# Kernel optimization log

Hardware: AMD Instinct MI355X
Metric: run time of the kernel (lower is better)

Reference implementation:

```python
import jax, jax.numpy as jnp
import numpy as np
import math

D_MODEL = 1024
N_HEADS = 16
D_HEAD = D_MODEL // N_HEADS


def setup_inputs() -> dict:
    key = jax.random.key(0)
    k_x, k_wqkv, k_bqkv, k_wp, k_bp = jax.random.split(key, 5)
    B, T = 2, 2048
    s = 1.0 / math.sqrt(D_MODEL)
    return {
        "x": jax.random.normal(k_x, (B, T, D_MODEL), dtype=jnp.float32),
        "W_qkv": jax.random.uniform(k_wqkv, (D_MODEL, 3 * D_MODEL), minval=-s, maxval=s, dtype=jnp.float32),
        "b_qkv": jax.random.uniform(k_bqkv, (3 * D_MODEL,), minval=-s, maxval=s, dtype=jnp.float32),
        "W_proj": jax.random.uniform(k_wp, (D_MODEL, D_MODEL), minval=-s, maxval=s, dtype=jnp.float32),
        "b_proj": jax.random.uniform(k_bp, (D_MODEL,), minval=-s, maxval=s, dtype=jnp.float32),
    }


def reference(x, W_qkv, b_qkv, W_proj, b_proj):
    B, T, C = x.shape
    qkv = x @ W_qkv + b_qkv                      # [B,T,3C]
    qkv = qkv.reshape(B, T, 3, N_HEADS, D_HEAD)
    qkv = jnp.transpose(qkv, (2, 0, 3, 1, 4))     # [3,B,H,T,dh]
    q, k, v = qkv[0], qkv[1], qkv[2]
    scale = math.sqrt(D_HEAD)
    attn = jnp.einsum('bhqd,bhkd->bhqk', q, k) / scale  # [B,H,T,T]
    causal = jnp.tril(jnp.ones((T, T), dtype=bool))
    attn = jnp.where(causal, attn, -jnp.inf)
    attn = jax.nn.softmax(attn, axis=-1)
    out = jnp.einsum('bhqk,bhkd->bhqd', attn, v)  # [B,H,T,dh]
    out = jnp.transpose(out, (0, 2, 1, 3)).reshape(B, T, C)
    return out @ W_proj + b_proj
```

## Files before the change

### kernel.cpp

```cpp
#include <hip/hip_runtime.h>

#define B_    2
#define T_    2048
#define C_    1024
#define H_    16
#define DH_   64
#define M_    (B_ * T_)
#define NQKV  (3 * C_)

typedef __bf16 bf16;
typedef __bf16 bf16x4 __attribute__((ext_vector_type(4)));
typedef __bf16 bf16x8 __attribute__((ext_vector_type(8)));
typedef float  f32x4  __attribute__((ext_vector_type(4)));

__device__ __forceinline__ void async16(const void* g, void* l) {
  __builtin_amdgcn_global_load_lds(
      (const __attribute__((address_space(1))) void*)g,
      (__attribute__((address_space(3))) void*)l, 16, 0, 0);
}

__global__ __launch_bounds__(256) void cvt_bf16_k(const float* __restrict__ in,
                                                  bf16* __restrict__ out) {
  const int i = (blockIdx.x * 256 + threadIdx.x) * 4;
  float4 v = *(const float4*)(in + i);
  bf16x4 o;
  o[0] = (bf16)v.x; o[1] = (bf16)v.y; o[2] = (bf16)v.z; o[3] = (bf16)v.w;
  *(bf16x4*)(out + i) = o;
}

__global__ __launch_bounds__(256) void transpose_cvt(const float* __restrict__ in,
                                                     bf16* __restrict__ out,
                                                     int R, int C) {
  __shared__ float tile[32][33];
  const int c0 = blockIdx.x * 32, r0 = blockIdx.y * 32;
  const int tx = threadIdx.x, ty = threadIdx.y;
#pragma unroll
  for (int j = 0; j < 4; j++)
    tile[ty + j * 8][tx] = in[(size_t)(r0 + ty + j * 8) * C + c0 + tx];
  __syncthreads();
#pragma unroll
  for (int j = 0; j < 4; j++)
    out[(size_t)(c0 + ty + j * 8) * R + r0 + tx] = (bf16)tile[tx][ty + j * 8];
}

template <int EPI, int BM>
__global__ __launch_bounds__(256) void gemm_k(
    const bf16* __restrict__ A, const bf16* __restrict__ Bt,
    const float* __restrict__ bias, float* __restrict__ outF,
    bf16* __restrict__ qb, bf16* __restrict__ kb, bf16* __restrict__ vtb) {
  constexpr int K = 1024;
  constexpr int MI = BM / 32;
  __shared__ alignas(16) bf16 As[BM * 64];
  __shared__ alignas(16) bf16 Bs[128 * 64];
  const int tid = threadIdx.x;
  const int lane = tid & 63, wv = tid >> 6;
  const int l15 = lane & 15, quad = lane >> 4;
  const int wm = (wv >> 1) * (BM / 2), wn = (wv & 1) * 64;
  const int m0 = blockIdx.x * BM, n0 = blockIdx.y * 128;

  f32x4 acc[MI][4] = {};

  const int srow = tid >> 3;
  const int sgb = ((tid & 7) ^ (srow & 7)) * 8;
  const bf16* ga = A + (size_t)(m0 + srow) * K + sgb;
  const bf16* gb = Bt + (size_t)(n0 + srow) * K + sgb;
  const int swz = l15 & 7;

  for (int it = 0; it < K / 64; ++it) {
    const int k0 = it * 64;
#pragma unroll
    for (int c = 0; c < BM / 32; c++)
      async16(ga + k0 + (size_t)(c * 32) * K, As + tid * 8 + c * 2048);
#pragma unroll
    for (int c = 0; c < 4; c++)
      async16(gb + k0 + (size_t)(c * 32) * K, Bs + tid * 8 + c * 2048);
    __syncthreads();
    bf16x8 af[2][MI], bfr[2][4];
#pragma unroll
    for (int kb = 0; kb < 2; kb++) {
#pragma unroll
      for (int i = 0; i < MI; i++)
        af[kb][i] = *(const bf16x8*)(As + (wm + i * 16 + l15) * 64 +
                                     (((kb * 4 + quad) ^ swz) << 3));
#pragma unroll
      for (int j = 0; j < 4; j++)
        bfr[kb][j] = *(const bf16x8*)(Bs + (wn + j * 16 + l15) * 64 +
                                      (((kb * 4 + quad) ^ swz) << 3));
    }
#pragma unroll
    for (int kb = 0; kb < 2; kb++)
#pragma unroll
      for (int i = 0; i < MI; i++)
#pragma unroll
        for (int j = 0; j < 4; j++)
          acc[i][j] = __builtin_amdgcn_mfma_f32_16x16x32_bf16(
              af[kb][i], bfr[kb][j], acc[i][j], 0, 0, 0);
    __syncthreads();
  }

#pragma unroll
  for (int i = 0; i < MI; i++) {
#pragma unroll
    for (int j = 0; j < 4; j++) {
      const int gcol = n0 + wn + j * 16 + l15;
      const float bv = bias[gcol];
#pragma unroll
      for (int r = 0; r < 4; r++) {
        const int grow = m0 + wm + i * 16 + quad * 4 + r;
        float v = acc[i][j][r] + bv;
        if constexpr (EPI == 0) {
          const int which = gcol >> 10;
          const int hn = gcol & 1023;
          const int h = hn >> 6, d = hn & 63;
          const int bb = grow >> 11, t = grow & 2047;
          const int head = bb * 16 + h;
          if (which == 0)
            qb[head * 131072 + t * 64 + d] = (bf16)(v * 0.1803368801f);
          else if (which == 1)
            kb[head * 131072 + t * 64 + d] = (bf16)v;
          else
            vtb[head * 131072 + d * 2048 + t] = (bf16)v;
        } else {
          outF[(size_t)grow * 1024 + gcol] = v;
        }
      }
    }
  }
}

__global__ __launch_bounds__(512, 2) void attn_k(const bf16* __restrict__ Q,
                                                 const bf16* __restrict__ K,
                                                 const bf16* __restrict__ Vt,
                                                 bf16* __restrict__ O) {
  __shared__ alignas(16) bf16 Ks[2][128 * 64];
  __shared__ alignas(16) bf16 Vs[2][64 * 128];
  __shared__ alignas(16) bf16 Ps[8][16 * 128];
  const int tid = threadIdx.x, lane = tid & 63, wv = tid >> 6;
  const int l15 = lane & 15, quad = lane >> 4;

  const int b = blockIdx.x;
  const int bh = (b & 7) | ((b >> 6) << 3);
  const int xpair = (b >> 3) & 7;

  const bf16* Qb = Q + (size_t)bh * 131072;
  const bf16* Kb = K + (size_t)bh * 131072;
  const bf16* Vb = Vt + (size_t)bh * 131072;

  const int krow = tid >> 3;
  const int kg = (tid & 7) ^ (krow & 7);
  const bf16* gk = Kb + krow * 64 + kg * 8;
  const int vrow = tid >> 4;
  const int vg = (tid & 15) ^ (vrow & 15);
  const bf16* gv = Vb + vrow * 2048 + vg * 8;

  const int swz7 = l15 & 7;
  bf16* Pw = Ps[wv];
  const int bb = bh >> 4, h = bh & 15;

  for (int t = 0; t < 2; ++t) {
    const int qJ = t ? (15 - xpair) : xpair;
    const int q0 = qJ * 128;
    const int nIter = qJ + 1;
    const int q = q0 + wv * 16 + l15;

    bf16x8 aq0 = *(const bf16x8*)(Qb + q * 64 + quad * 8);
    bf16x8 aq1 = *(const bf16x8*)(Qb + q * 64 + 32 + quad * 8);

    f32x4 o[4] = {};
    float m = -3.0e38f, lsum = 0.f;

    __syncthreads();
    async16(gk, &Ks[0][tid * 8]);
    async16(gk + 64 * 64, &Ks[0][tid * 8 + 4096]);
    async16(gv, &Vs[0][tid * 8]);
    async16(gv + 32 * 2048, &Vs[0][tid * 8 + 4096]);

    for (int it = 0; it < nIter; ++it) {
      __syncthreads();
      const bf16* Kc = Ks[it & 1];
      const bf16* Vc = Vs[it & 1];

      bf16x8 kf[2][8];
#pragma unroll
      for (int kc = 0; kc < 2; kc++)
#pragma unroll
        for (int nf = 0; nf < 8; nf++)
          kf[kc][nf] = *(const bf16x8*)(Kc + (nf * 16 + l15) * 64 +
                                        (((kc * 4 + quad) ^ swz7) << 3));

      if (it + 1 < nIter) {
        const int kt1 = (it + 1) * 128;
        const int nb = (it + 1) & 1;
        async16(gk + kt1 * 64, &Ks[nb][tid * 8]);
        async16(gk + kt1 * 64 + 64 * 64, &Ks[nb][tid * 8 + 4096]);
        async16(gv + kt1, &Vs[nb][tid * 8]);
        async16(gv + kt1 + 32 * 2048, &Vs[nb][tid * 8 + 4096]);
      }

      f32x4 s[8] = {};
#pragma unroll
      for (int kc = 0; kc < 2; kc++) {
        bf16x8 a = kc ? aq1 : aq0;
#pragma unroll
        for (int nf = 0; nf < 8; nf++)
          s[nf] = __builtin_amdgcn_mfma_f32_16x16x32_bf16(kf[kc][nf], a, s[nf], 0, 0, 0);
      }

      if (it == nIter - 1) {
#pragma unroll
        for (int nf = 0; nf < 8; nf++)
#pragma unroll
          for (int r = 0; r < 4; r++) {
            const int kt = it * 128 + nf * 16 + quad * 4 + r;
            if (kt > q) s[nf][r] = -3.0e38f;
          }
      }

      float mx = s[0][0];
#pragma unroll
      for (int nf = 0; nf < 8; nf++)
#pragma unroll
        for (int r = 0; r < 4; r++) mx = fmaxf(mx, s[nf][r]);
      mx = fmaxf(mx, __shfl_xor(mx, 16));
      mx = fmaxf(mx, __shfl_xor(mx, 32));
      const float mnew = fmaxf(m, mx);
      const float alpha = __builtin_amdgcn_exp2f(m - mnew);
      m = mnew;
      float ts = 0.f;
      bf16x4 p4[8];
#pragma unroll
      for (int nf = 0; nf < 8; nf++)
#pragma unroll
        for (int r = 0; r < 4; r++) {
          const float pv = __builtin_amdgcn_exp2f(s[nf][r] - mnew);
          ts += pv;
          p4[nf][r] = (bf16)pv;
        }
      ts += __shfl_xor(ts, 16);
      ts += __shfl_xor(ts, 32);
      lsum = lsum * alpha + ts;
#pragma unroll
      for (int nf = 0; nf < 4; nf++)
#pragma unroll
        for (int r = 0; r < 4; r++) o[nf][r] *= alpha;

#pragma unroll
      for (int nf = 0; nf < 8; nf++)
        *(bf16x4*)(Pw + l15 * 128 + ((((nf << 1) | (quad >> 1)) ^ l15) << 3) +
                   ((quad & 1) << 2)) = p4[nf];

      bf16x8 pb[4];
#pragma unroll
      for (int kc = 0; kc < 4; kc++)
        pb[kc] = *(const bf16x8*)(Pw + l15 * 128 + (((kc * 4 + quad) ^ l15) << 3));

#pragma unroll
      for (int kc = 0; kc < 4; kc++)
#pragma unroll
        for (int nf = 0; nf < 4; nf++) {
          bf16x8 vf = *(const bf16x8*)(Vc + (nf * 16 + l15) * 128 +
                                       (((kc * 4 + quad) ^ l15) << 3));
          o[nf] = __builtin_amdgcn_mfma_f32_16x16x32_bf16(vf, pb[kc], o[nf], 0, 0, 0);
        }
    }

    const float inv = 1.0f / lsum;
#pragma unroll
    for (int nf = 0; nf < 4; nf++) {
      bf16x4 ov;
#pragma unroll
      for (int r = 0; r < 4; r++) ov[r] = (bf16)(o[nf][r] * inv);
      *(bf16x4*)(O + (size_t)(bb * 2048 + q) * 1024 + h * 64 + nf * 16 + quad * 4) = ov;
    }
  }
}

extern "C" void kernel_launch(void* const* d_in, const int* in_sizes, int n_in,
                              void* d_out, int out_size, void* d_ws, size_t ws_size,
                              hipStream_t stream) {
  const float* x     = (const float*)d_in[0];
  const float* Wqkv  = (const float*)d_in[1];
  const float* bqkv  = (const float*)d_in[2];
  const float* Wproj = (const float*)d_in[3];
  const float* bproj = (const float*)d_in[4];
  float* out = (float*)d_out;

  char* p = (char*)d_ws;
  bf16* xbf    = (bf16*)p; p += (size_t)M_ * C_ * 2;
  bf16* wqkvT  = (bf16*)p; p += (size_t)NQKV * C_ * 2;
  bf16* wprojT = (bf16*)p; p += (size_t)C_ * C_ * 2;
  bf16* Qb     = (bf16*)p; p += (size_t)M_ * C_ * 2;
  bf16* Kb     = (bf16*)p; p += (size_t)M_ * C_ * 2;
  bf16* Vtb    = (bf16*)p; p += (size_t)M_ * C_ * 2;
  bf16* AO     = (bf16*)p;

  cvt_bf16_k<<<M_ * C_ / 1024, 256, 0, stream>>>(x, xbf);
  transpose_cvt<<<dim3(NQKV / 32, C_ / 32), dim3(32, 8), 0, stream>>>(Wqkv, wqkvT, C_, NQKV);
  transpose_cvt<<<dim3(C_ / 32, C_ / 32), dim3(32, 8), 0, stream>>>(Wproj, wprojT, C_, C_);

  gemm_k<0, 128><<<dim3(M_ / 128, NQKV / 128), 256, 0, stream>>>(
      xbf, wqkvT, bqkv, nullptr, Qb, Kb, Vtb);

  attn_k<<<256, 512, 0, stream>>>(Qb, Kb, Vtb, AO);

  gemm_k<1, 64><<<dim3(M_ / 64, C_ / 128), 256, 0, stream>>>(
      AO, wprojT, bproj, out, nullptr, nullptr, nullptr);
}
```

Baseline: 173.0 us.

## Split attention blocks per query tile and shrink LDS for higher occupancy

The attention kernel now launches one block per query tile instead of looping over a paired tile, doubling the grid and dropping the balanced-pair loop. LDS use is cut by single-buffering K (with an extra barrier mid-QK so the next K tile can be prefetched after the first half of the dot product) and by halving the per-wave P staging buffer, which is processed in two halves. Launch bounds ask for 4 blocks per CU to raise occupancy. The cost is an extra barrier per iteration, less K prefetch overlap, and tighter register limits that may cause spills. Work per block is also less balanced across blocks than with the paired scheme.

```diff
diff --git a/kernel.cpp b/kernel.cpp
--- a/kernel.cpp
+++ b/kernel.cpp
@@ -77,24 +77,24 @@
     __syncthreads();
     bf16x8 af[2][MI], bfr[2][4];
 #pragma unroll
-    for (int kb = 0; kb < 2; kb++) {
+    for (int kk = 0; kk < 2; kk++) {
 #pragma unroll
       for (int i = 0; i < MI; i++)
-        af[kb][i] = *(const bf16x8*)(As + (wm + i * 16 + l15) * 64 +
-                                     (((kb * 4 + quad) ^ swz) << 3));
+        af[kk][i] = *(const bf16x8*)(As + (wm + i * 16 + l15) * 64 +
+                                     (((kk * 4 + quad) ^ swz) << 3));
 #pragma unroll
       for (int j = 0; j < 4; j++)
-        bfr[kb][j] = *(const bf16x8*)(Bs + (wn + j * 16 + l15) * 64 +
-                                      (((kb * 4 + quad) ^ swz) << 3));
-    }
-#pragma unroll
-    for (int kb = 0; kb < 2; kb++)
+        bfr[kk][j] = *(const bf16x8*)(Bs + (wn + j * 16 + l15) * 64 +
+                                      (((kk * 4 + quad) ^ swz) << 3));
+    }
+#pragma unroll
+    for (int kk = 0; kk < 2; kk++)
 #pragma unroll
       for (int i = 0; i < MI; i++)
 #pragma unroll
         for (int j = 0; j < 4; j++)
           acc[i][j] = __builtin_amdgcn_mfma_f32_16x16x32_bf16(
-              af[kb][i], bfr[kb][j], acc[i][j], 0, 0, 0);
+              af[kk][i], bfr[kk][j], acc[i][j], 0, 0, 0);
     __syncthreads();
   }
 
@@ -128,19 +128,23 @@
   }
 }
 
-__global__ __launch_bounds__(512, 2) void attn_k(const bf16* __restrict__ Q,
+__global__ __launch_bounds__(512, 4) void attn_k(const bf16* __restrict__ Q,
                                                  const bf16* __restrict__ K,
                                                  const bf16* __restrict__ Vt,
                                                  bf16* __restrict__ O) {
-  __shared__ alignas(16) bf16 Ks[2][128 * 64];
+  __shared__ alignas(16) bf16 Ks[128 * 64];
   __shared__ alignas(16) bf16 Vs[2][64 * 128];
-  __shared__ alignas(16) bf16 Ps[8][16 * 128];
+  __shared__ alignas(16) bf16 Ps[8][16 * 64];
   const int tid = threadIdx.x, lane = tid & 63, wv = tid >> 6;
   const int l15 = lane & 15, quad = lane >> 4;
 
   const int b = blockIdx.x;
-  const int bh = (b & 7) | ((b >> 6) << 3);
-  const int xpair = (b >> 3) & 7;
+  const int sH = b >> 8, i = b & 255;
+  const int bh = (i & 7) | (((i >> 3) & 3) << 3);
+  const int x = i >> 5;
+  const int qJ = sH ? (15 - x) : x;
+  const int q0 = qJ * 128;
+  const int nIter = qJ + 1;
 
   const bf16* Qb = Q + (size_t)bh * 131072;
   const bf16* Kb = K + (size_t)bh * 131072;
@@ -157,121 +161,115 @@
   bf16* Pw = Ps[wv];
   const int bb = bh >> 4, h = bh & 15;
 
-  for (int t = 0; t < 2; ++t) {
-    const int qJ = t ? (15 - xpair) : xpair;
-    const int q0 = qJ * 128;
-    const int nIter = qJ + 1;
-    const int q = q0 + wv * 16 + l15;
-
-    bf16x8 aq0 = *(const bf16x8*)(Qb + q * 64 + quad * 8);
-    bf16x8 aq1 = *(const bf16x8*)(Qb + q * 64 + 32 + quad * 8);
-
-    f32x4 o[4] = {};
-    float m = -3.0e38f, lsum = 0.f;
-
+  const int q = q0 + wv * 16 + l15;
+  bf16x8 aq0 = *(const bf16x8*)(Qb + q * 64 + quad * 8);
+  bf16x8 aq1 = *(const bf16x8*)(Qb + q * 64 + 32 + quad * 8);
+
+  f32x4 o[4] = {};
+  float m = -3.0e38f, lsum = 0.f;
+
+  async16(gk, &Ks[tid * 8]);
+  async16(gk + 64 * 64, &Ks[tid * 8 + 4096]);
+  async16(gv, &Vs[0][tid * 8]);
+  async16(gv + 32 * 2048, &Vs[0][tid * 8 + 4096]);
+
+  for (int it = 0; it < nIter; ++it) {
     __syncthreads();
-    async16(gk, &Ks[0][tid * 8]);
-    async16(gk + 64 * 64, &Ks[0][tid * 8 + 4096]);
-    async16(gv, &Vs[0][tid * 8]);
-    async16(gv + 32 * 2048, &Vs[0][tid * 8 + 4096]);
-
-    for (int it = 0; it < nIter; ++it) {
-      __syncthreads();
-      const bf16* Kc = Ks[it & 1];
-      const bf16* Vc = Vs[it & 1];
-
-      bf16x8 kf[2][8];
-#pragma unroll
-      for (int kc = 0; kc < 2; kc++)
-#pragma unroll
-        for (int nf = 0; nf < 8; nf++)
-          kf[kc][nf] = *(const bf16x8*)(Kc + (nf * 16 + l15) * 64 +
-                                        (((kc * 4 + quad) ^ swz7) << 3));
-
-      if (it + 1 < nIter) {
-        const int kt1 = (it + 1) * 128;
-        const int nb = (it + 1) & 1;
-        async16(gk + kt1 * 64, &Ks[nb][tid * 8]);
-        async16(gk + kt1 * 64 + 64 * 64, &Ks[nb][tid * 8 + 4096]);
-        async16(gv + kt1, &Vs[nb][tid * 8]);
-        async16(gv + kt1 + 32 * 2048, &Vs[nb][tid * 8 + 4096]);
+    const bf16* Vc = Vs[it & 1];
+
+    bf16x8 kf0[8], kf1[8];
+#pragma unroll
+    for (int nf = 0; nf < 8; nf++)
+      kf0[nf] = *(const bf16x8*)(Ks + (nf * 16 + l15) * 64 + ((quad ^ swz7) << 3));
+#pragma unroll
+    for (int nf = 0; nf < 8; nf++)
+      kf1[nf] = *(const bf16x8*)(Ks + (nf * 16 + l15) * 64 + (((4 + quad) ^ swz7) << 3));
+
+    f32x4 s[8] = {};
+#pragma unroll
+    for (int nf = 0; nf < 8; nf++)
+      s[nf] = __builtin_amdgcn_mfma_f32_16x16x32_bf16(kf0[nf], aq0, s[nf], 0, 0, 0);
+
+    __syncthreads();
+    if (it + 1 < nIter) {
+      const int kt1 = (it + 1) * 128;
+      async16(gk + kt1 * 64, &Ks[tid * 8]);
+      async16(gk + kt1 * 64 + 64 * 64, &Ks[tid * 8 + 4096]);
+      async16(gv + kt1, &Vs[(it + 1) & 1][tid * 8]);
+      async16(gv + kt1 + 32 * 2048, &Vs[(it + 1) & 1][tid * 8 + 4096]);
+    }
+
+#pragma unroll
+    for (int nf = 0; nf < 8; nf++)
+      s[nf] = __builtin_amdgcn_mfma_f32_16x16x32_bf16(kf1[nf], aq1, s[nf], 0, 0, 0);
+
+    if (it == nIter - 1) {
+#pragma unroll
+      for (int nf = 0; nf < 8; nf++)
+#pragma unroll
+        for (int r = 0; r < 4; r++) {
+          const int kt = it * 128 + nf * 16 + quad * 4 + r;
+          if (kt > q) s[nf][r] = -3.0e38f;
+        }
+    }
+
+    float mx = s[0][0];
+#pragma unroll
+    for (int nf = 0; nf < 8; nf++)
+#pragma unroll
+      for (int r = 0; r < 4; r++) mx = fmaxf(mx, s[nf][r]);
+    mx = fmaxf(mx, __shfl_xor(mx, 16));
+    mx = fmaxf(mx, __shfl_xor(mx, 32));
+    const float mnew = fmaxf(m, mx);
+    const float alpha = __builtin_amdgcn_exp2f(m - mnew);
+    m = mnew;
+    float ts = 0.f;
+    bf16x4 p4[8];
+#pragma unroll
+    for (int nf = 0; nf < 8; nf++)
+#pragma unroll
+      for (int r = 0; r < 4; r++) {
+        const float pv = __builtin_amdgcn_exp2f(s[nf][r] - mnew);
+        ts += pv;
+        p4[nf][r] = (bf16)pv;
       }
-
-      f32x4 s[8] = {};
+    ts += __shfl_xor(ts, 16);
+    ts += __shfl_xor(ts, 32);
+    lsum = lsum * alpha + ts;
+#pragma unroll
+    for (int nf = 0; nf < 4; nf++)
+#pragma unroll
+      for (int r = 0; r < 4; r++) o[nf][r] *= alpha;
+
+#pragma unroll
+    for (int half = 0; half < 2; half++) {
+#pragma unroll
+      for (int nf = 0; nf < 4; nf++)
+        *(bf16x4*)(Pw + l15 * 64 + ((((nf << 1) | (quad >> 1)) ^ swz7) << 3) +
+                   ((quad & 1) << 2)) = p4[half * 4 + nf];
+      bf16x8 pb0 = *(const bf16x8*)(Pw + l15 * 64 + ((quad ^ swz7) << 3));
+      bf16x8 pb1 = *(const bf16x8*)(Pw + l15 * 64 + (((4 + quad) ^ swz7) << 3));
 #pragma unroll
       for (int kc = 0; kc < 2; kc++) {
-        bf16x8 a = kc ? aq1 : aq0;
-#pragma unroll
-        for (int nf = 0; nf < 8; nf++)
-          s[nf] = __builtin_amdgcn_mfma_f32_16x16x32_bf16(kf[kc][nf], a, s[nf], 0, 0, 0);
-      }
-
-      if (it == nIter - 1) {
-#pragma unroll
-        for (int nf = 0; nf < 8; nf++)
-#pragma unroll
-          for (int r = 0; r < 4; r++) {
-            const int kt = it * 128 + nf * 16 + quad * 4 + r;
-            if (kt > q) s[nf][r] = -3.0e38f;
-          }
-      }
-
-      float mx = s[0][0];
-#pragma unroll
-      for (int nf = 0; nf < 8; nf++)
-#pragma unroll
-        for (int r = 0; r < 4; r++) mx = fmaxf(mx, s[nf][r]);
-      mx = fmaxf(mx, __shfl_xor(mx, 16));
-      mx = fmaxf(mx, __shfl_xor(mx, 32));
-      const float mnew = fmaxf(m, mx);
-      const float alpha = __builtin_amdgcn_exp2f(m - mnew);
-      m = mnew;
-      float ts = 0.f;
-      bf16x4 p4[8];
-#pragma unroll
-      for (int nf = 0; nf < 8; nf++)
-#pragma unroll
-        for (int r = 0; r < 4; r++) {
-          const float pv = __builtin_amdgcn_exp2f(s[nf][r] - mnew);
-          ts += pv;
-          p4[nf][r] = (bf16)pv;
-        }
-      ts += __shfl_xor(ts, 16);
-      ts += __shfl_xor(ts, 32);
-      lsum = lsum * alpha + ts;
-#pragma unroll
-      for (int nf = 0; nf < 4; nf++)
-#pragma unroll
-        for (int r = 0; r < 4; r++) o[nf][r] *= alpha;
-
-#pragma unroll
-      for (int nf = 0; nf < 8; nf++)
-        *(bf16x4*)(Pw + l15 * 128 + ((((nf << 1) | (quad >> 1)) ^ l15) << 3) +
-                   ((quad & 1) << 2)) = p4[nf];
-
-      bf16x8 pb[4];
-#pragma unroll
-      for (int kc = 0; kc < 4; kc++)
-        pb[kc] = *(const bf16x8*)(Pw + l15 * 128 + (((kc * 4 + quad) ^ l15) << 3));
-
-#pragma unroll
-      for (int kc = 0; kc < 4; kc++)
+        bf16x8 pb = kc ? pb1 : pb0;
+        const int kcg = half * 2 + kc;
 #pragma unroll
         for (int nf = 0; nf < 4; nf++) {
           bf16x8 vf = *(const bf16x8*)(Vc + (nf * 16 + l15) * 128 +
-                                       (((kc * 4 + quad) ^ l15) << 3));
-          o[nf] = __builtin_amdgcn_mfma_f32_16x16x32_bf16(vf, pb[kc], o[nf], 0, 0, 0);
+                                       (((kcg * 4 + quad) ^ l15) << 3));
+          o[nf] = __builtin_amdgcn_mfma_f32_16x16x32_bf16(vf, pb, o[nf], 0, 0, 0);
         }
-    }
-
-    const float inv = 1.0f / lsum;
-#pragma unroll
-    for (int nf = 0; nf < 4; nf++) {
-      bf16x4 ov;
-#pragma unroll
-      for (int r = 0; r < 4; r++) ov[r] = (bf16)(o[nf][r] * inv);
-      *(bf16x4*)(O + (size_t)(bb * 2048 + q) * 1024 + h * 64 + nf * 16 + quad * 4) = ov;
-    }
+      }
+    }
+  }
+
+  const float inv = 1.0f / lsum;
+#pragma unroll
+  for (int nf = 0; nf < 4; nf++) {
+    bf16x4 ov;
+#pragma unroll
+    for (int r = 0; r < 4; r++) ov[r] = (bf16)(o[nf][r] * inv);
+    *(bf16x4*)(O + (size_t)(bb * 2048 + q) * 1024 + h * 64 + nf * 16 + quad * 4) = ov;
   }
 }
 
@@ -301,7 +299,7 @@
   gemm_k<0, 128><<<dim3(M_ / 128, NQKV / 128), 256, 0, stream>>>(
       xbf, wqkvT, bqkv, nullptr, Qb, Kb, Vtb);
 
-  attn_k<<<256, 512, 0, stream>>>(Qb, Kb, Vtb, AO);
+  attn_k<<<512, 512, 0, stream>>>(Qb, Kb, Vtb, AO);
 
   gemm_k<1, 64><<<dim3(M_ / 64, C_ / 128), 256, 0, stream>>>(
       AO, wprojT, bproj, out, nullptr, nullptr, nullptr);
```

After: 173.8 us. No clear change (+0.4%).
